# Optimization experiments

Hardware: AMD Instinct MI355X
Metric: run time of the kernel (lower is better)

## Reference

```python
import jax, jax.numpy as jnp
import numpy as np

N_SRC = 131072
N_DST = 65536
N_EDGES = 524288
D_IN = 128
D_OUT = 128


def setup_inputs() -> dict:
    key = jax.random.key(0)
    k1, k2, k3, k4, k5 = jax.random.split(key, 5)
    feat = jax.random.normal(k1, (N_SRC, D_IN), dtype=jnp.float32)
    # xavier_uniform-ish scale for the two projections
    lim = float(np.sqrt(6.0 / (D_IN + D_OUT))) * np.sqrt(2.0)
    W_self = jax.random.uniform(k2, (D_IN, D_OUT), jnp.float32, -lim, lim)
    W_neigh = jax.random.uniform(k3, (D_IN, D_OUT), jnp.float32, -lim, lim)
    b_self = jnp.zeros((D_OUT,), jnp.float32)
    b_neigh = jnp.zeros((D_OUT,), jnp.float32)
    src_idx = jax.random.randint(k4, (N_EDGES,), 0, N_SRC, dtype=jnp.int32)
    dst_idx = jnp.sort(jax.random.randint(k5, (N_EDGES,), 0, N_DST, dtype=jnp.int32))
    return {
        "feat": feat,
        "W_self": W_self,
        "b_self": b_self,
        "W_neigh": W_neigh,
        "b_neigh": b_neigh,
        "src_idx": src_idx,
        "dst_idx": dst_idx,
        "num_row": N_DST,
    }


def reference(feat, W_self, b_self, W_neigh, b_neigh, src_idx, dst_idx, num_row):
    # h_self: destination-node features (first num_row rows)
    h_self = feat[:num_row, :]                              # [num_row, D_IN]
    # csrmm: mean aggregation of source neighbor features per destination row
    gathered = feat[src_idx]                                # [E, D_IN]
    neigh_sum = jax.ops.segment_sum(gathered, dst_idx, num_segments=num_row)
    deg = jax.ops.segment_sum(jnp.ones_like(dst_idx, dtype=feat.dtype), dst_idx,
                              num_segments=num_row)
    h_neigh = neigh_sum / jnp.maximum(deg, 1.0)[:, None]    # [num_row, D_IN]
    # dual linear projections
    rst = (h_self @ W_self + b_self) + (h_neigh @ W_neigh + b_neigh)
    return rst
```

## Files before the change

kernel.cpp:

```cpp
#include <hip/hip_runtime.h>
#include <hip/hip_bf16.h>

#define N_SRC   131072
#define N_DST   65536
#define D       128

typedef __bf16 bf16x8 __attribute__((ext_vector_type(8)));
typedef float  f32x4  __attribute__((ext_vector_type(4)));

#define CONV_BLOCKS 8192
#define W_BLOCKS    64

__global__ __launch_bounds__(256) void prep_kernel(
    const float* __restrict__ feat,
    const int*   __restrict__ dst, int n_edges, int n_bnd_blocks,
    const float* __restrict__ W_self, const float* __restrict__ W_neigh,
    __bf16* __restrict__ feat_bf,
    int*    __restrict__ row_start,
    __bf16* __restrict__ Wt_self, __bf16* __restrict__ Wt_neigh)
{
    const int b = blockIdx.x;
    const int t = threadIdx.x;

    if (b < CONV_BLOCKS) {
        const size_t i0 = ((size_t)b * 256 + t) * 8;
        const float4 a0 = *(const float4*)&feat[i0];
        const float4 a1 = *(const float4*)&feat[i0 + 4];
        bf16x8 o;
        o[0] = (__bf16)a0.x; o[1] = (__bf16)a0.y; o[2] = (__bf16)a0.z; o[3] = (__bf16)a0.w;
        o[4] = (__bf16)a1.x; o[5] = (__bf16)a1.y; o[6] = (__bf16)a1.z; o[7] = (__bf16)a1.w;
        *(bf16x8*)&feat_bf[i0] = o;
    } else if (b < CONV_BLOCKS + n_bnd_blocks) {
        const int e = (b - CONV_BLOCKS) * 256 + t;
        if (e < n_edges) {
            const int d    = dst[e];
            const int prev = (e == 0) ? -1 : dst[e - 1];
            for (int r = prev + 1; r <= d; ++r) row_start[r] = e;
            if (e == n_edges - 1)
                for (int r = d + 1; r <= N_DST; ++r) row_start[r] = n_edges;
        }
    } else {
        const int wb  = b - CONV_BLOCKS - n_bnd_blocks;
        const int idx = wb * 256 + t;
        const int k = idx >> 7, n = idx & 127;
        Wt_self [n * D + k] = (__bf16)W_self [k * D + n];
        Wt_neigh[n * D + k] = (__bf16)W_neigh[k * D + n];
    }
}

#define MTILE 64
#define MREP  2
#define NBLK  2

__global__ __launch_bounds__(512) void fused_kernel(
    const __bf16* __restrict__ feat_bf,
    const int*    __restrict__ src,
    const int*    __restrict__ row_start,
    const __bf16* __restrict__ Wt_self,
    const __bf16* __restrict__ Wt_neigh,
    const float*  __restrict__ b_self,
    const float*  __restrict__ b_neigh,
    float*        __restrict__ out)
{
    __shared__ __align__(16) __bf16 hs[MTILE * D];
    __shared__ int rs[MTILE + 1];
    char* hsb = (char*)hs;

    const int t     = threadIdx.x;
    const int tile0 = blockIdx.x * MTILE;

    if (t <= MTILE) rs[t] = row_start[tile0 + t];
    __syncthreads();

    {
        const int g    = t >> 4;
        const int lane = t & 15;
        const int cb   = lane * 16;

        #pragma unroll
        for (int rr = 0; rr < MTILE / 32; ++rr) {
            const int rloc = rr * 32 + g;
            const int s0 = rs[rloc];
            const int s1 = rs[rloc + 1];

            float acc[8] = {0.f, 0.f, 0.f, 0.f, 0.f, 0.f, 0.f, 0.f};

            int idx[8];
            #pragma unroll
            for (int j = 0; j < 8; ++j) {
                int e = s0 + j; e = e < s1 ? e : s1 - 1; e = e > 0 ? e : 0;
                idx[j] = src[e];
            }

            for (int base = s0; base < s1; base += 8) {
                bf16x8 v[8];
                #pragma unroll
                for (int j = 0; j < 8; ++j)
                    v[j] = *(const bf16x8*)((const char*)feat_bf + (size_t)idx[j] * (D * 2) + cb);
                int nidx[8];
                #pragma unroll
                for (int j = 0; j < 8; ++j) {
                    int e = base + 8 + j; e = e < s1 ? e : s1 - 1; e = e > 0 ? e : 0;
                    nidx[j] = src[e];
                }
                #pragma unroll
                for (int j = 0; j < 8; ++j) {
                    const float m = (base + j < s1) ? 1.0f : 0.0f;
                    #pragma unroll
                    for (int c = 0; c < 8; ++c)
                        acc[c] = fmaf(m, (float)v[j][c], acc[c]);
                }
                #pragma unroll
                for (int j = 0; j < 8; ++j) idx[j] = nidx[j];
            }

            const float inv = 1.0f / fmaxf((float)(s1 - s0), 1.0f);
            bf16x8 o;
            #pragma unroll
            for (int c = 0; c < 8; ++c) o[c] = (__bf16)(acc[c] * inv);
            *(bf16x8*)(hsb + rloc * 256 + (cb ^ ((rloc & 7) << 4))) = o;
        }
    }

    const int w     = t >> 6;
    const int l     = t & 63;
    const int m16   = l & 15;
    const int quad  = l >> 4;
    const int kb    = quad * 8;
    const int wrow  = w & 1;
    const int wcol  = w >> 1;
    const int rowloc0 = wrow * (16 * MREP);
    const int rowbase = tile0 + rowloc0;
    const int colbase = wcol * (16 * NBLK);

    f32x4 acc[MREP][NBLK];
    #pragma unroll
    for (int rp = 0; rp < MREP; ++rp)
        #pragma unroll
        for (int nb = 0; nb < NBLK; ++nb)
            acc[rp][nb] = (f32x4){0.f, 0.f, 0.f, 0.f};

    #pragma unroll
    for (int ks = 0; ks < 4; ++ks) {
        bf16x8 afrag[MREP];
        #pragma unroll
        for (int rp = 0; rp < MREP; ++rp)
            afrag[rp] = *(const bf16x8*)&feat_bf[(size_t)(rowbase + rp * 16 + m16) * D + ks * 32 + kb];
        #pragma unroll
        for (int nb = 0; nb < NBLK; ++nb) {
            const bf16x8 bfrag = *(const bf16x8*)&Wt_self[(size_t)(colbase + nb * 16 + m16) * D + ks * 32 + kb];
            #pragma unroll
            for (int rp = 0; rp < MREP; ++rp)
                acc[rp][nb] = __builtin_amdgcn_mfma_f32_16x16x32_bf16(
                    afrag[rp], bfrag, acc[rp][nb], 0, 0, 0);
        }
    }

    __syncthreads();

    #pragma unroll
    for (int ks = 0; ks < 4; ++ks) {
        bf16x8 afrag[MREP];
        #pragma unroll
        for (int rp = 0; rp < MREP; ++rp) {
            const int rloc  = rowloc0 + rp * 16 + m16;
            const int cbyte = (ks * 32 + kb) * 2;
            afrag[rp] = *(const bf16x8*)(hsb + rloc * 256 + (cbyte ^ ((rloc & 7) << 4)));
        }
        #pragma unroll
        for (int nb = 0; nb < NBLK; ++nb) {
            const bf16x8 bfrag = *(const bf16x8*)&Wt_neigh[(size_t)(colbase + nb * 16 + m16) * D + ks * 32 + kb];
            #pragma unroll
            for (int rp = 0; rp < MREP; ++rp)
                acc[rp][nb] = __builtin_amdgcn_mfma_f32_16x16x32_bf16(
                    afrag[rp], bfrag, acc[rp][nb], 0, 0, 0);
        }
    }

    #pragma unroll
    for (int nb = 0; nb < NBLK; ++nb) {
        const int col  = colbase + nb * 16 + m16;
        const float bias = b_self[col] + b_neigh[col];
        #pragma unroll
        for (int rp = 0; rp < MREP; ++rp) {
            const int orow0 = rowbase + rp * 16 + quad * 4;
            #pragma unroll
            for (int r = 0; r < 4; ++r)
                out[(size_t)(orow0 + r) * D + col] = acc[rp][nb][r] + bias;
        }
    }
}

extern "C" void kernel_launch(void* const* d_in, const int* in_sizes, int n_in,
                              void* d_out, int out_size, void* d_ws, size_t ws_size,
                              hipStream_t stream)
{
    const float* feat    = (const float*)d_in[0];
    const float* W_self  = (const float*)d_in[1];
    const float* b_self  = (const float*)d_in[2];
    const float* W_neigh = (const float*)d_in[3];
    const float* b_neigh = (const float*)d_in[4];
    const int*   src_idx = (const int*)d_in[5];
    const int*   dst_idx = (const int*)d_in[6];
    const int n_edges = in_sizes[5];

    char* ws = (char*)d_ws;
    __bf16* feat_bf  = (__bf16*)ws;
    int*    row_start = (int*)(feat_bf + (size_t)N_SRC * D);
    __bf16* Wt_self  = (__bf16*)(row_start + N_DST + 16);
    __bf16* Wt_neigh = Wt_self + D * D;

    const int n_bnd = (n_edges + 255) / 256;
    prep_kernel<<<CONV_BLOCKS + n_bnd + W_BLOCKS, 256, 0, stream>>>(
        feat, dst_idx, n_edges, n_bnd, W_self, W_neigh,
        feat_bf, row_start, Wt_self, Wt_neigh);

    fused_kernel<<<N_DST / MTILE, 512, 0, stream>>>(
        feat_bf, src_idx, row_start, Wt_self, Wt_neigh,
        b_self, b_neigh, (float*)d_out);
}
```

Measured before the change: 162.3 us.

## Gather fp32 features directly and drop the bf16 conversion pass; enlarge tiles

```diff
diff --git a/kernel.cpp b/kernel.cpp
--- a/kernel.cpp
+++ b/kernel.cpp
@@ -8,30 +8,19 @@
 typedef __bf16 bf16x8 __attribute__((ext_vector_type(8)));
 typedef float  f32x4  __attribute__((ext_vector_type(4)));
 
-#define CONV_BLOCKS 8192
-#define W_BLOCKS    64
+#define W_BLOCKS 64
 
 __global__ __launch_bounds__(256) void prep_kernel(
-    const float* __restrict__ feat,
     const int*   __restrict__ dst, int n_edges, int n_bnd_blocks,
     const float* __restrict__ W_self, const float* __restrict__ W_neigh,
-    __bf16* __restrict__ feat_bf,
     int*    __restrict__ row_start,
     __bf16* __restrict__ Wt_self, __bf16* __restrict__ Wt_neigh)
 {
     const int b = blockIdx.x;
     const int t = threadIdx.x;
 
-    if (b < CONV_BLOCKS) {
-        const size_t i0 = ((size_t)b * 256 + t) * 8;
-        const float4 a0 = *(const float4*)&feat[i0];
-        const float4 a1 = *(const float4*)&feat[i0 + 4];
-        bf16x8 o;
-        o[0] = (__bf16)a0.x; o[1] = (__bf16)a0.y; o[2] = (__bf16)a0.z; o[3] = (__bf16)a0.w;
-        o[4] = (__bf16)a1.x; o[5] = (__bf16)a1.y; o[6] = (__bf16)a1.z; o[7] = (__bf16)a1.w;
-        *(bf16x8*)&feat_bf[i0] = o;
-    } else if (b < CONV_BLOCKS + n_bnd_blocks) {
-        const int e = (b - CONV_BLOCKS) * 256 + t;
+    if (b < n_bnd_blocks) {
+        const int e = b * 256 + t;
         if (e < n_edges) {
             const int d    = dst[e];
             const int prev = (e == 0) ? -1 : dst[e - 1];
@@ -40,7 +29,7 @@
                 for (int r = d + 1; r <= N_DST; ++r) row_start[r] = n_edges;
         }
     } else {
-        const int wb  = b - CONV_BLOCKS - n_bnd_blocks;
+        const int wb  = b - n_bnd_blocks;
         const int idx = wb * 256 + t;
         const int k = idx >> 7, n = idx & 127;
         Wt_self [n * D + k] = (__bf16)W_self [k * D + n];
@@ -48,14 +37,14 @@
     }
 }
 
-#define MTILE 64
+#define MTILE 128
 #define MREP  2
-#define NBLK  2
+#define NBLK  4
 
 __global__ __launch_bounds__(512) void fused_kernel(
-    const __bf16* __restrict__ feat_bf,
-    const int*    __restrict__ src,
-    const int*    __restrict__ row_start,
+    const float* __restrict__ feat,
+    const int*   __restrict__ src,
+    const int*   __restrict__ row_start,
     const __bf16* __restrict__ Wt_self,
     const __bf16* __restrict__ Wt_neigh,
     const float*  __restrict__ b_self,
@@ -75,6 +64,7 @@
     {
         const int g    = t >> 4;
         const int lane = t & 15;
+        const int c0   = lane * 8;
         const int cb   = lane * 16;
 
         #pragma unroll
@@ -93,10 +83,13 @@
             }
 
             for (int base = s0; base < s1; base += 8) {
-                bf16x8 v[8];
-                #pragma unroll
-                for (int j = 0; j < 8; ++j)
-                    v[j] = *(const bf16x8*)((const char*)feat_bf + (size_t)idx[j] * (D * 2) + cb);
+                f32x4 va[8], vb[8];
+                #pragma unroll
+                for (int j = 0; j < 8; ++j) {
+                    const float* p = feat + (size_t)idx[j] * D + c0;
+                    va[j] = *(const f32x4*)p;
+                    vb[j] = *(const f32x4*)(p + 4);
+                }
                 int nidx[8];
                 #pragma unroll
                 for (int j = 0; j < 8; ++j) {
@@ -107,8 +100,11 @@
                 for (int j = 0; j < 8; ++j) {
                     const float m = (base + j < s1) ? 1.0f : 0.0f;
                     #pragma unroll
-                    for (int c = 0; c < 8; ++c)
-                        acc[c] = fmaf(m, (float)v[j][c], acc[c]);
+                    for (int c = 0; c < 4; ++c)
+                        acc[c] = fmaf(m, va[j][c], acc[c]);
+                    #pragma unroll
+                    for (int c = 0; c < 4; ++c)
+                        acc[4 + c] = fmaf(m, vb[j][c], acc[4 + c]);
                 }
                 #pragma unroll
                 for (int j = 0; j < 8; ++j) idx[j] = nidx[j];
@@ -127,11 +123,11 @@
     const int m16   = l & 15;
     const int quad  = l >> 4;
     const int kb    = quad * 8;
-    const int wrow  = w & 1;
-    const int wcol  = w >> 1;
+    const int wrow  = w & 3;
+    const int whalf = w >> 2;
     const int rowloc0 = wrow * (16 * MREP);
     const int rowbase = tile0 + rowloc0;
-    const int colbase = wcol * (16 * NBLK);
+    const int colbase = whalf * 64;
 
     f32x4 acc[MREP][NBLK];
     #pragma unroll
@@ -144,8 +140,15 @@
     for (int ks = 0; ks < 4; ++ks) {
         bf16x8 afrag[MREP];
         #pragma unroll
-        for (int rp = 0; rp < MREP; ++rp)
-            afrag[rp] = *(const bf16x8*)&feat_bf[(size_t)(rowbase + rp * 16 + m16) * D + ks * 32 + kb];
+        for (int rp = 0; rp < MREP; ++rp) {
+            const float* ap = &feat[(size_t)(rowbase + rp * 16 + m16) * D + ks * 32 + kb];
+            const f32x4 x0 = *(const f32x4*)ap;
+            const f32x4 x1 = *(const f32x4*)(ap + 4);
+            #pragma unroll
+            for (int c = 0; c < 4; ++c) afrag[rp][c]     = (__bf16)x0[c];
+            #pragma unroll
+            for (int c = 0; c < 4; ++c) afrag[rp][4 + c] = (__bf16)x1[c];
+        }
         #pragma unroll
         for (int nb = 0; nb < NBLK; ++nb) {
             const bf16x8 bfrag = *(const bf16x8*)&Wt_self[(size_t)(colbase + nb * 16 + m16) * D + ks * 32 + kb];
@@ -205,17 +208,16 @@
     const int n_edges = in_sizes[5];
 
     char* ws = (char*)d_ws;
-    __bf16* feat_bf  = (__bf16*)ws;
-    int*    row_start = (int*)(feat_bf + (size_t)N_SRC * D);
-    __bf16* Wt_self  = (__bf16*)(row_start + N_DST + 16);
-    __bf16* Wt_neigh = Wt_self + D * D;
+    int*    row_start = (int*)ws;
+    __bf16* Wt_self   = (__bf16*)(row_start + N_DST + 16);
+    __bf16* Wt_neigh  = Wt_self + D * D;
 
     const int n_bnd = (n_edges + 255) / 256;
-    prep_kernel<<<CONV_BLOCKS + n_bnd + W_BLOCKS, 256, 0, stream>>>(
-        feat, dst_idx, n_edges, n_bnd, W_self, W_neigh,
-        feat_bf, row_start, Wt_self, Wt_neigh);
+    prep_kernel<<<n_bnd + W_BLOCKS, 256, 0, stream>>>(
+        dst_idx, n_edges, n_bnd, W_self, W_neigh,
+        row_start, Wt_self, Wt_neigh);
 
     fused_kernel<<<N_DST / MTILE, 512, 0, stream>>>(
-        feat_bf, src_idx, row_start, Wt_self, Wt_neigh,
+        feat, src_idx, row_start, Wt_self, Wt_neigh,
         b_self, b_neigh, (float*)d_out);
 }
```

Result: faster. 157.2 us (-3.2%).
